# Optimization experiments

Hardware: AMD Instinct MI355X
Metric: run time of the kernel (lower is better)

## Reference

```python
import jax, jax.numpy as jnp
import numpy as np

K = 8
NUM_BLOCKS = 12

def knn_idx(xyz, k):
    # xyz: (B,3,N). kNN in Euclidean space (self included), like gutil.group.
    sq = jnp.sum(xyz * xyz, axis=1)                      # (B,N)
    inner = jnp.einsum('bdn,bdm->bnm', xyz, xyz)         # (B,N,N)
    dist = sq[:, :, None] - 2.0 * inner + sq[:, None, :]
    _, idx = jax.lax.top_k(-dist, k)                     # (B,N,k)
    return idx

def gather_neighbors(points, idx):
    # points: (B,d,N), idx: (B,N,k) -> grouped (B,d,k,N)  [gutil.group_point]
    g = jax.vmap(lambda p, i: p[:, i])(points, idx)      # (B,d,N,k)
    return jnp.transpose(g, (0, 1, 3, 2))

def setup_inputs() -> dict:
    key = jax.random.key(0)
    ks = jax.random.split(key, 6)
    B, N, D = 4, 4096, 128
    return {
        'xyz': jax.random.normal(ks[0], (B, 3, N), dtype=jnp.float32),
        'points': jax.random.normal(ks[1], (B, D, N), dtype=jnp.float32),
        'conv_w1': jax.random.normal(ks[2], (NUM_BLOCKS, D, D), dtype=jnp.float32) * 0.05,
        'conv_w2': jax.random.normal(ks[3], (NUM_BLOCKS, D, D), dtype=jnp.float32) * 0.05,
        'w_center': jax.random.normal(ks[4], (6, D), dtype=jnp.float32) * 0.05,
        'w_neighbor': jax.random.normal(ks[5], (6, D), dtype=jnp.float32) * 0.05,
    }

def reference(xyz, points, conv_w1, conv_w2, w_center, w_neighbor):
    # kNN indices depend only on xyz -> computed once (idx==0 branch in torch).
    idx = knn_idx(xyz, K)
    inv = 1.0 / (K + 1)
    for i in range(NUM_BLOCKS):
        shortcut = points
        p = jax.nn.relu(points)                              # (B,d,N)
        grouped = gather_neighbors(p, idx)                   # (B,d,K,N)
        center = jnp.einsum('oi,bin->bon', conv_w1[i], p)    # 1x1 conv on center
        gnn_sum = jnp.einsum('oi,bikn->bon', conv_w2[i], grouped)  # conv + sum over K
        # mean over concat([center(1), grouped(K)]) along neighbor dim + residual
        points = (center + gnn_sum) * inv + shortcut
        if i == NUM_BLOCKS - 1:
            pxyz = jnp.einsum('oi,bin->bon', w_center, p)            # (B,6,N)
            gxyz_sum = jnp.einsum('oi,bikn->bon', w_neighbor, grouped)
            new_xyz = (pxyz + gxyz_sum) * inv                        # (B,6,N)
            B, _, N = xyz.shape
            new_xyz = new_xyz.reshape(B, 3, 2, N) + xyz[:, :, None, :]
            new_xyz = new_xyz.reshape(B, 3, 2 * N)
            return (new_xyz, points)
```

## Files before the change

kernel.cpp:

```cpp
#include <hip/hip_runtime.h>
#include <math.h>

#define BB 4
#define NN 4096
#define DD 128
#define KK 8
#define NBLK 12

typedef __attribute__((ext_vector_type(8))) short short8;
typedef __attribute__((ext_vector_type(4))) float f32x4;

__device__ inline ushort bf16_rn(float x) {
    uint u = __float_as_uint(x);
    u = (u + 0x7FFFu + ((u >> 16) & 1u)) >> 16;
    return (ushort)u;
}
__device__ inline float bf16_f(ushort h) { return __uint_as_float(((uint)h) << 16); }

__global__ __launch_bounds__(512) void knn_kernel(const float* __restrict__ xyz,
                                                  int* __restrict__ idx) {
    __shared__ float xs[NN], ys[NN], zs[NN], sq[NN];
    const int b = blockIdx.y;
    const float* xb = xyz + (size_t)b * 3 * NN;
    for (int i = threadIdx.x; i < NN; i += 512) {
        float x = xb[i], y = xb[NN + i], z = xb[2 * NN + i];
        xs[i] = x; ys[i] = y; zs[i] = z;
        sq[i] = __fadd_rn(__fadd_rn(__fmul_rn(x, x), __fmul_rn(y, y)),
                          __fmul_rn(z, z));
    }
    __syncthreads();

    const int wave = threadIdx.x >> 6;
    const int lane = threadIdx.x & 63;
    const int n = blockIdx.x * 8 + wave;
    const float qx = xs[n], qy = ys[n], qz = zs[n], qsq = sq[n];

    float d[KK];
    int id[KK];
#pragma unroll
    for (int j = 0; j < KK; ++j) { d[j] = INFINITY; id[j] = -1; }

    for (int j = 0; j < NN / 256; ++j) {
        const int m0 = j * 256 + lane * 4;
        const float4 vx = *(const float4*)&xs[m0];
        const float4 vy = *(const float4*)&ys[m0];
        const float4 vz = *(const float4*)&zs[m0];
        const float4 vq = *(const float4*)&sq[m0];
#pragma unroll
        for (int e = 0; e < 4; ++e) {
            const float cx = (&vx.x)[e], cy = (&vy.x)[e], cz = (&vz.x)[e];
            const float cq = (&vq.x)[e];
            float inner = __fadd_rn(__fadd_rn(__fmul_rn(qx, cx),
                                              __fmul_rn(qy, cy)),
                                    __fmul_rn(qz, cz));
            float dist = __fadd_rn(__fsub_rn(qsq, __fmul_rn(2.0f, inner)), cq);
            if (dist < d[KK - 1]) {
                d[KK - 1] = dist; id[KK - 1] = m0 + e;
#pragma unroll
                for (int t = KK - 1; t > 0; --t) {
                    if (d[t] < d[t - 1]) {
                        float td = d[t]; d[t] = d[t - 1]; d[t - 1] = td;
                        int ti = id[t]; id[t] = id[t - 1]; id[t - 1] = ti;
                    }
                }
            }
        }
    }

    int out[KK];
#pragma unroll
    for (int it = 0; it < KK; ++it) {
        float hd = d[0];
        int hi = id[0];
#pragma unroll
        for (int s = 32; s; s >>= 1) {
            float od = __shfl_xor(hd, s, 64);
            int oi = __shfl_xor(hi, s, 64);
            if (od < hd || (od == hd && oi < hi)) { hd = od; hi = oi; }
        }
        out[it] = hi;
        if (hd == d[0] && hi == id[0]) {
#pragma unroll
            for (int t = 0; t < KK - 1; ++t) { d[t] = d[t + 1]; id[t] = id[t + 1]; }
            d[KK - 1] = INFINITY; id[KK - 1] = -1;
        }
    }

    if (lane == 0) {
        int* op = idx + ((size_t)b * NN + n) * KK;
        *(int4*)op       = make_int4(out[0], out[1], out[2], out[3]);
        *(int4*)(op + 4) = make_int4(out[4], out[5], out[6], out[7]);
    }
}

__global__ __launch_bounds__(256) void prep_w(const float* __restrict__ w1,
                                              const float* __restrict__ w2,
                                              ushort* __restrict__ whi,
                                              ushort* __restrict__ wlo) {
    const int e = blockIdx.x * 256 + threadIdx.x;
    const int l = e >> 15;
    const int rem = e & 32767;
    const int r = rem >> 8;
    const int k = rem & 255;
    float w = (k < 128) ? w1[((size_t)l * 128 + r) * 128 + k]
                        : w2[((size_t)l * 128 + r) * 128 + (k - 128)];
    ushort h = bf16_rn(w);
    whi[e] = h;
    wlo[e] = bf16_rn(w - bf16_f(h));
}

__global__ __launch_bounds__(256) void transpose_pts(const float* __restrict__ pts,
                                                     float* __restrict__ ptsT) {
    __shared__ float t[32][33];
    const int b = blockIdx.z;
    const int c0 = blockIdx.y * 32;
    const int n0 = blockIdx.x * 32;
    const int tx = threadIdx.x & 31;
    const int ty = threadIdx.x >> 5;
#pragma unroll
    for (int q = 0; q < 4; ++q)
        t[ty + 8 * q][tx] = pts[((size_t)b * DD + c0 + ty + 8 * q) * NN + n0 + tx];
    __syncthreads();
#pragma unroll
    for (int q = 0; q < 4; ++q)
        ptsT[((size_t)b * NN + n0 + ty + 8 * q) * DD + c0 + tx] = t[tx][ty + 8 * q];
}

__global__ __launch_bounds__(512, 4) void fused_block(const float* __restrict__ ptsT_in,
                                                      const int* __restrict__ idx,
                                                      const ushort* __restrict__ whi,
                                                      const ushort* __restrict__ wlo,
                                                      float* __restrict__ ptsT_out,
                                                      float* __restrict__ out_std,
                                                      const float* __restrict__ wc,
                                                      const float* __restrict__ wn,
                                                      const float* __restrict__ xyz,
                                                      float* __restrict__ out_xyz,
                                                      const int last) {
    __shared__ __align__(16) char xt[32768];
    __shared__ float sc[32][132];
    char* xt_hi = xt;
    char* xt_lo = xt + 16384;

    const int bid = blockIdx.x;
    const int xcd = bid & 7;
    const int b = xcd >> 1;
    const int colbase = (((xcd & 1) << 6) + (bid >> 3)) * 32;

    const int w = threadIdx.x >> 6;
    const int lane = threadIdx.x & 63;
    const int half = lane >> 5;
    const int l32 = lane & 31;
    const int choff = 4 * l32;
    const int row0 = w * 4;

    const float* baseT = ptsT_in + (size_t)b * NN * DD;

    const int iv = idx[((size_t)b * NN + colbase + row0) * KK + (lane & 31)];

    const int ln15 = lane & 15;
    const int kl = lane >> 4;

#pragma unroll
    for (int i = 0; i < 2; ++i) {
        const int n_loc = row0 + 2 * i + half;
        const int n = colbase + n_loc;

        int nb[KK];
#pragma unroll
        for (int j = 0; j < KK; ++j) nb[j] = __shfl(iv, (2 * i + half) * 8 + j, 64);

        const float4 c4 = *(const float4*)(baseT + (size_t)n * DD + choff);
        float4 u[KK];
#pragma unroll
        for (int j = 0; j < KK; ++j)
            u[j] = *(const float4*)(baseT + (size_t)nb[j] * DD + choff);

        float g0 = 0.f, g1 = 0.f, g2 = 0.f, g3 = 0.f;
#pragma unroll
        for (int j = 0; j < KK; ++j) {
            g0 += fmaxf(u[j].x, 0.f);
            g1 += fmaxf(u[j].y, 0.f);
            g2 += fmaxf(u[j].z, 0.f);
            g3 += fmaxf(u[j].w, 0.f);
        }
        const float p0 = fmaxf(c4.x, 0.f);
        const float p1 = fmaxf(c4.y, 0.f);
        const float p2 = fmaxf(c4.z, 0.f);
        const float p3 = fmaxf(c4.w, 0.f);

        *(float4*)&sc[n_loc][choff] = c4;

        ushort ph0 = bf16_rn(p0), ph1 = bf16_rn(p1), ph2 = bf16_rn(p2), ph3 = bf16_rn(p3);
        ushort pl0 = bf16_rn(p0 - bf16_f(ph0)), pl1 = bf16_rn(p1 - bf16_f(ph1));
        ushort pl2 = bf16_rn(p2 - bf16_f(ph2)), pl3 = bf16_rn(p3 - bf16_f(ph3));
        ushort gh0 = bf16_rn(g0), gh1 = bf16_rn(g1), gh2 = bf16_rn(g2), gh3 = bf16_rn(g3);
        ushort gl0 = bf16_rn(g0 - bf16_f(gh0)), gl1 = bf16_rn(g1 - bf16_f(gh1));
        ushort gl2 = bf16_rn(g2 - bf16_f(gh2)), gl3 = bf16_rn(g3 - bf16_f(gh3));

        const int gP = l32 >> 1;
        const int sub = (l32 & 1) << 3;
        const int byP = n_loc * 512 + ((gP ^ (n_loc & 7)) << 4) + sub;
        const int byG = n_loc * 512 + (((16 + gP) ^ (n_loc & 7)) << 4) + sub;

        *(unsigned long long*)(xt_hi + byP) =
            (unsigned long long)ph0 | ((unsigned long long)ph1 << 16) |
            ((unsigned long long)ph2 << 32) | ((unsigned long long)ph3 << 48);
        *(unsigned long long*)(xt_lo + byP) =
            (unsigned long long)pl0 | ((unsigned long long)pl1 << 16) |
            ((unsigned long long)pl2 << 32) | ((unsigned long long)pl3 << 48);
        *(unsigned long long*)(xt_hi + byG) =
            (unsigned long long)gh0 | ((unsigned long long)gh1 << 16) |
            ((unsigned long long)gh2 << 32) | ((unsigned long long)gh3 << 48);
        *(unsigned long long*)(xt_lo + byG) =
            (unsigned long long)gl0 | ((unsigned long long)gl1 << 16) |
            ((unsigned long long)gl2 << 32) | ((unsigned long long)gl3 << 48);

        if (last) {
            float s0, s1, s2, s3, s4, s5;
            {
                const int c0 = choff, c1 = choff + 1, c2 = choff + 2, c3 = choff + 3;
                s0 = p0 * wc[0 * 128 + c0] + p1 * wc[0 * 128 + c1] + p2 * wc[0 * 128 + c2] + p3 * wc[0 * 128 + c3]
                   + g0 * wn[0 * 128 + c0] + g1 * wn[0 * 128 + c1] + g2 * wn[0 * 128 + c2] + g3 * wn[0 * 128 + c3];
                s1 = p0 * wc[1 * 128 + c0] + p1 * wc[1 * 128 + c1] + p2 * wc[1 * 128 + c2] + p3 * wc[1 * 128 + c3]
                   + g0 * wn[1 * 128 + c0] + g1 * wn[1 * 128 + c1] + g2 * wn[1 * 128 + c2] + g3 * wn[1 * 128 + c3];
                s2 = p0 * wc[2 * 128 + c0] + p1 * wc[2 * 128 + c1] + p2 * wc[2 * 128 + c2] + p3 * wc[2 * 128 + c3]
                   + g0 * wn[2 * 128 + c0] + g1 * wn[2 * 128 + c1] + g2 * wn[2 * 128 + c2] + g3 * wn[2 * 128 + c3];
                s3 = p0 * wc[3 * 128 + c0] + p1 * wc[3 * 128 + c1] + p2 * wc[3 * 128 + c2] + p3 * wc[3 * 128 + c3]
                   + g0 * wn[3 * 128 + c0] + g1 * wn[3 * 128 + c1] + g2 * wn[3 * 128 + c2] + g3 * wn[3 * 128 + c3];
                s4 = p0 * wc[4 * 128 + c0] + p1 * wc[4 * 128 + c1] + p2 * wc[4 * 128 + c2] + p3 * wc[4 * 128 + c3]
                   + g0 * wn[4 * 128 + c0] + g1 * wn[4 * 128 + c1] + g2 * wn[4 * 128 + c2] + g3 * wn[4 * 128 + c3];
                s5 = p0 * wc[5 * 128 + c0] + p1 * wc[5 * 128 + c1] + p2 * wc[5 * 128 + c2] + p3 * wc[5 * 128 + c3]
                   + g0 * wn[5 * 128 + c0] + g1 * wn[5 * 128 + c1] + g2 * wn[5 * 128 + c2] + g3 * wn[5 * 128 + c3];
            }
#pragma unroll
            for (int st = 16; st; st >>= 1) {
                s0 += __shfl_xor(s0, st, 64);
                s1 += __shfl_xor(s1, st, 64);
                s2 += __shfl_xor(s2, st, 64);
                s3 += __shfl_xor(s3, st, 64);
                s4 += __shfl_xor(s4, st, 64);
                s5 += __shfl_xor(s5, st, 64);
            }
            if (l32 < 6) {
                float v = s0;
                v = (l32 == 1) ? s1 : v;
                v = (l32 == 2) ? s2 : v;
                v = (l32 == 3) ? s3 : v;
                v = (l32 == 4) ? s4 : v;
                v = (l32 == 5) ? s5 : v;
                const int dd = l32 >> 1, h = l32 & 1;
                const float xv = xyz[((size_t)b * 3 + dd) * NN + n];
                out_xyz[(((size_t)b * 3 + dd) * 2 + h) * NN + n] =
                    v * (1.0f / 9.0f) + xv;
            }
        }
    }
    __syncthreads();

    const int wrow = w * 16 + ln15;
    f32x4 acc[2] = {};
#pragma unroll
    for (int ks = 0; ks < 8; ++ks) {
        const short8 a_hi = *(const short8*)(whi + (size_t)wrow * 256 + ks * 32 + kl * 8);
        const short8 a_lo = *(const short8*)(wlo + (size_t)wrow * 256 + ks * 32 + kl * 8);
        short8 bfh[2], bfl[2];
#pragma unroll
        for (int nt = 0; nt < 2; ++nt) {
            const int n_loc = nt * 16 + ln15;
            const int by = n_loc * 512 + (((ks * 4 + kl) ^ (n_loc & 7)) << 4);
            bfh[nt] = *(const short8*)(xt_hi + by);
            bfl[nt] = *(const short8*)(xt_lo + by);
        }
#pragma unroll
        for (int nt = 0; nt < 2; ++nt) {
            acc[nt] = __builtin_amdgcn_mfma_f32_16x16x32_bf16(a_hi, bfh[nt], acc[nt], 0, 0, 0);
            acc[nt] = __builtin_amdgcn_mfma_f32_16x16x32_bf16(a_hi, bfl[nt], acc[nt], 0, 0, 0);
            acc[nt] = __builtin_amdgcn_mfma_f32_16x16x32_bf16(a_lo, bfh[nt], acc[nt], 0, 0, 0);
        }
    }

    const float inv = 1.0f / 9.0f;
    const int orow = w * 16 + kl * 4;
#pragma unroll
    for (int nt = 0; nt < 2; ++nt) {
        const int nl = nt * 16 + ln15;
        const int n = colbase + nl;
        const float4 scv = *(const float4*)&sc[nl][orow];
        float v0 = acc[nt][0] * inv + scv.x;
        float v1 = acc[nt][1] * inv + scv.y;
        float v2 = acc[nt][2] * inv + scv.z;
        float v3 = acc[nt][3] * inv + scv.w;
        if (!last) {
            *(float4*)(ptsT_out + ((size_t)b * NN + n) * DD + orow) =
                make_float4(v0, v1, v2, v3);
        } else {
            out_std[((size_t)b * DD + orow + 0) * NN + n] = v0;
            out_std[((size_t)b * DD + orow + 1) * NN + n] = v1;
            out_std[((size_t)b * DD + orow + 2) * NN + n] = v2;
            out_std[((size_t)b * DD + orow + 3) * NN + n] = v3;
        }
    }
}

extern "C" void kernel_launch(void* const* d_in, const int* in_sizes, int n_in,
                              void* d_out, int out_size, void* d_ws, size_t ws_size,
                              hipStream_t stream) {
    const float* xyz    = (const float*)d_in[0];
    const float* points = (const float*)d_in[1];
    const float* w1     = (const float*)d_in[2];
    const float* w2     = (const float*)d_in[3];
    const float* wc     = (const float*)d_in[4];
    const float* wn     = (const float*)d_in[5];
    float* out = (float*)d_out;

    const size_t feat = (size_t)BB * DD * NN;
    char* ws = (char*)d_ws;
    int*    idx  = (int*)ws;
    ushort* whi  = (ushort*)(ws + 524288);
    ushort* wlo  = (ushort*)(ws + 524288 + 786432);
    float*  pT0  = (float*)(ws + 524288 + 2 * 786432);
    float*  pT1  = pT0 + feat;

    knn_kernel<<<dim3(NN / 8, BB), 512, 0, stream>>>(xyz, idx);
    prep_w<<<dim3(12 * 128 * 256 / 256), 256, 0, stream>>>(w1, w2, whi, wlo);
    transpose_pts<<<dim3(NN / 32, DD / 32, BB), 256, 0, stream>>>(points, pT0);

    float* out_pts = out + (size_t)BB * 3 * 2 * NN;
    float* bufs[2] = {pT0, pT1};
    for (int i = 0; i < NBLK; ++i) {
        const int last = (i == NBLK - 1);
        fused_block<<<dim3(512), 512, 0, stream>>>(
            bufs[i & 1], idx, whi + (size_t)i * 32768, wlo + (size_t)i * 32768,
            bufs[(i + 1) & 1], out_pts, wc, wn, xyz, out, last);
    }
}
```

Measured before the change: 296.3 us.

## Reorder points by Morton code so kNN gathers hit nearby rows

Adds a per-batch Morton-code bitonic sort of the points, then permutes the feature rows and the remapped kNN indices into spatial order. The 12 fused blocks then run in that order, and the final outputs are scattered back to original positions through the permutation. The aim is better cache locality for the neighbour gathers, since spatially close points now sit in nearby memory. In exchange it adds a single-block-per-batch sort, two permute kernels, an extra workspace buffer and non-coalesced scattered stores in the last block.

Result: slower. 325.6 us (+9.9%).

```diff
diff --git a/kernel.cpp b/kernel.cpp
--- a/kernel.cpp
+++ b/kernel.cpp
@@ -91,6 +91,75 @@
         *(int4*)op       = make_int4(out[0], out[1], out[2], out[3]);
         *(int4*)(op + 4) = make_int4(out[4], out[5], out[6], out[7]);
     }
+}
+
+__device__ inline uint expand10(uint v) {
+    v &= 0x3FFu;
+    v = (v | (v << 16)) & 0x030000FFu;
+    v = (v | (v << 8))  & 0x0300F00Fu;
+    v = (v | (v << 4))  & 0x030C30C3u;
+    v = (v | (v << 2))  & 0x09249249u;
+    return v;
+}
+
+__global__ __launch_bounds__(1024) void morton_sort(const float* __restrict__ xyz,
+                                                    int* __restrict__ perm,
+                                                    int* __restrict__ inv) {
+    __shared__ unsigned long long a[NN];
+    const int b = blockIdx.x;
+    const float* xb = xyz + (size_t)b * 3 * NN;
+    for (int i = threadIdx.x; i < NN; i += 1024) {
+        float x = xb[i], y = xb[NN + i], z = xb[2 * NN + i];
+        uint qx = (uint)fminf(fmaxf((x + 4.f) * 128.f, 0.f), 1023.f);
+        uint qy = (uint)fminf(fmaxf((y + 4.f) * 128.f, 0.f), 1023.f);
+        uint qz = (uint)fminf(fmaxf((z + 4.f) * 128.f, 0.f), 1023.f);
+        uint code = (expand10(qx) << 2) | (expand10(qy) << 1) | expand10(qz);
+        a[i] = ((unsigned long long)code << 32) | (uint)i;
+    }
+    __syncthreads();
+    for (int k = 2; k <= NN; k <<= 1) {
+        for (int j = k >> 1; j > 0; j >>= 1) {
+            for (int t = threadIdx.x; t < NN / 2; t += 1024) {
+                const int i = ((t & ~(j - 1)) << 1) | (t & (j - 1));
+                const int l = i | j;
+                const bool up = ((i & k) == 0);
+                unsigned long long ai = a[i], al = a[l];
+                if ((ai > al) == up) { a[i] = al; a[l] = ai; }
+            }
+            __syncthreads();
+        }
+    }
+    for (int i = threadIdx.x; i < NN; i += 1024) {
+        const int orig = (int)(a[i] & 0xFFFFFFFFu);
+        perm[b * NN + i] = orig;
+        inv[b * NN + orig] = i;
+    }
+}
+
+__global__ __launch_bounds__(256) void permute_idx(const int* __restrict__ idx,
+                                                   const int* __restrict__ perm,
+                                                   const int* __restrict__ inv,
+                                                   int* __restrict__ idxp) {
+    const int b = blockIdx.y;
+    const int n = blockIdx.x * 256 + threadIdx.x;
+    const int orig = perm[b * NN + n];
+    const int* src = idx + ((size_t)b * NN + orig) * KK;
+    const int* invb = inv + b * NN;
+    int* dst = idxp + ((size_t)b * NN + n) * KK;
+#pragma unroll
+    for (int k = 0; k < KK; ++k) dst[k] = invb[src[k]];
+}
+
+__global__ __launch_bounds__(256) void permute_rows(const float* __restrict__ src,
+                                                    const int* __restrict__ perm,
+                                                    float* __restrict__ dst) {
+    const int b = blockIdx.y;
+    const int w = threadIdx.x >> 6;
+    const int lane = threadIdx.x & 63;
+    const int n = blockIdx.x * 4 + w;
+    const int orig = perm[b * NN + n];
+    const float2 v = *(const float2*)(src + ((size_t)b * NN + orig) * DD + 2 * lane);
+    *(float2*)(dst + ((size_t)b * NN + n) * DD + 2 * lane) = v;
 }
 
 __global__ __launch_bounds__(256) void prep_w(const float* __restrict__ w1,
@@ -127,7 +196,7 @@
 }
 
 __global__ __launch_bounds__(512, 4) void fused_block(const float* __restrict__ ptsT_in,
-                                                      const int* __restrict__ idx,
+                                                      const int* __restrict__ idxp,
                                                       const ushort* __restrict__ whi,
                                                       const ushort* __restrict__ wlo,
                                                       float* __restrict__ ptsT_out,
@@ -136,6 +205,7 @@
                                                       const float* __restrict__ wn,
                                                       const float* __restrict__ xyz,
                                                       float* __restrict__ out_xyz,
+                                                      const int* __restrict__ perm,
                                                       const int last) {
     __shared__ __align__(16) char xt[32768];
     __shared__ float sc[32][132];
@@ -156,7 +226,7 @@
 
     const float* baseT = ptsT_in + (size_t)b * NN * DD;
 
-    const int iv = idx[((size_t)b * NN + colbase + row0) * KK + (lane & 31)];
+    const int iv = idxp[((size_t)b * NN + colbase + row0) * KK + (lane & 31)];
 
     const int ln15 = lane & 15;
     const int kl = lane >> 4;
@@ -249,9 +319,10 @@
                 v = (l32 == 3) ? s3 : v;
                 v = (l32 == 4) ? s4 : v;
                 v = (l32 == 5) ? s5 : v;
+                const int norig = perm[b * NN + n];
                 const int dd = l32 >> 1, h = l32 & 1;
-                const float xv = xyz[((size_t)b * 3 + dd) * NN + n];
-                out_xyz[(((size_t)b * 3 + dd) * 2 + h) * NN + n] =
+                const float xv = xyz[((size_t)b * 3 + dd) * NN + norig];
+                out_xyz[(((size_t)b * 3 + dd) * 2 + h) * NN + norig] =
                     v * (1.0f / 9.0f) + xv;
             }
         }
@@ -295,10 +366,11 @@
             *(float4*)(ptsT_out + ((size_t)b * NN + n) * DD + orow) =
                 make_float4(v0, v1, v2, v3);
         } else {
-            out_std[((size_t)b * DD + orow + 0) * NN + n] = v0;
-            out_std[((size_t)b * DD + orow + 1) * NN + n] = v1;
-            out_std[((size_t)b * DD + orow + 2) * NN + n] = v2;
-            out_std[((size_t)b * DD + orow + 3) * NN + n] = v3;
+            const int norig = perm[b * NN + n];
+            out_std[((size_t)b * DD + orow + 0) * NN + norig] = v0;
+            out_std[((size_t)b * DD + orow + 1) * NN + norig] = v1;
+            out_std[((size_t)b * DD + orow + 2) * NN + norig] = v2;
+            out_std[((size_t)b * DD + orow + 3) * NN + norig] = v3;
         }
     }
 }
@@ -316,22 +388,29 @@
 
     const size_t feat = (size_t)BB * DD * NN;
     char* ws = (char*)d_ws;
-    int*    idx  = (int*)ws;
-    ushort* whi  = (ushort*)(ws + 524288);
-    ushort* wlo  = (ushort*)(ws + 524288 + 786432);
-    float*  pT0  = (float*)(ws + 524288 + 2 * 786432);
-    float*  pT1  = pT0 + feat;
+    int*    idx   = (int*)(ws + 0);
+    int*    idxp  = (int*)(ws + 524288);
+    int*    perm  = (int*)(ws + 1048576);
+    int*    inv   = (int*)(ws + 1114112);
+    ushort* whi   = (ushort*)(ws + 1179648);
+    ushort* wlo   = (ushort*)(ws + 1966080);
+    float*  pT0   = (float*)(ws + 2752512);
+    float*  pT1   = pT0 + feat;
+    float*  pTt   = pT1 + feat;
 
     knn_kernel<<<dim3(NN / 8, BB), 512, 0, stream>>>(xyz, idx);
+    morton_sort<<<dim3(BB), 1024, 0, stream>>>(xyz, perm, inv);
     prep_w<<<dim3(12 * 128 * 256 / 256), 256, 0, stream>>>(w1, w2, whi, wlo);
-    transpose_pts<<<dim3(NN / 32, DD / 32, BB), 256, 0, stream>>>(points, pT0);
+    transpose_pts<<<dim3(NN / 32, DD / 32, BB), 256, 0, stream>>>(points, pTt);
+    permute_rows<<<dim3(NN / 4, BB), 256, 0, stream>>>(pTt, perm, pT0);
+    permute_idx<<<dim3(NN / 256, BB), 256, 0, stream>>>(idx, perm, inv, idxp);
 
     float* out_pts = out + (size_t)BB * 3 * 2 * NN;
     float* bufs[2] = {pT0, pT1};
     for (int i = 0; i < NBLK; ++i) {
         const int last = (i == NBLK - 1);
         fused_block<<<dim3(512), 512, 0, stream>>>(
-            bufs[i & 1], idx, whi + (size_t)i * 32768, wlo + (size_t)i * 32768,
-            bufs[(i + 1) & 1], out_pts, wc, wn, xyz, out, last);
-    }
-}
+            bufs[i & 1], idxp, whi + (size_t)i * 32768, wlo + (size_t)i * 32768,
+            bufs[(i + 1) & 1], out_pts, wc, wn, xyz, out, perm, last);
+    }
+}
```

## Halve fused block column tile to 16 and recompute squared norms in kNN

Applied to the files above, without the earlier changes.

Each fused_block workgroup now covers 16 points instead of 32, so the grid doubles to 1024 workgroups and LDS use per workgroup halves. Each workgroup does one gather iteration and one MFMA column tile instead of two. The aim is more parallelism and occupancy across the GPU, at the cost of reloading the per-block weight fragments twice as often. Separately, the kNN kernel drops the shared squared-norm array and recomputes the norms in the inner loop, trading extra ALU work for less LDS traffic.

After: 346.5 us. 17.0% more time.

```diff
diff --git a/kernel.cpp b/kernel.cpp
--- a/kernel.cpp
+++ b/kernel.cpp
@@ -19,21 +19,22 @@
 
 __global__ __launch_bounds__(512) void knn_kernel(const float* __restrict__ xyz,
                                                   int* __restrict__ idx) {
-    __shared__ float xs[NN], ys[NN], zs[NN], sq[NN];
+    __shared__ float xs[NN], ys[NN], zs[NN];
     const int b = blockIdx.y;
     const float* xb = xyz + (size_t)b * 3 * NN;
     for (int i = threadIdx.x; i < NN; i += 512) {
-        float x = xb[i], y = xb[NN + i], z = xb[2 * NN + i];
-        xs[i] = x; ys[i] = y; zs[i] = z;
-        sq[i] = __fadd_rn(__fadd_rn(__fmul_rn(x, x), __fmul_rn(y, y)),
-                          __fmul_rn(z, z));
+        xs[i] = xb[i];
+        ys[i] = xb[NN + i];
+        zs[i] = xb[2 * NN + i];
     }
     __syncthreads();
 
     const int wave = threadIdx.x >> 6;
     const int lane = threadIdx.x & 63;
     const int n = blockIdx.x * 8 + wave;
-    const float qx = xs[n], qy = ys[n], qz = zs[n], qsq = sq[n];
+    const float qx = xs[n], qy = ys[n], qz = zs[n];
+    const float qsq = __fadd_rn(__fadd_rn(__fmul_rn(qx, qx), __fmul_rn(qy, qy)),
+                                __fmul_rn(qz, qz));
 
     float d[KK];
     int id[KK];
@@ -45,11 +46,12 @@
         const float4 vx = *(const float4*)&xs[m0];
         const float4 vy = *(const float4*)&ys[m0];
         const float4 vz = *(const float4*)&zs[m0];
-        const float4 vq = *(const float4*)&sq[m0];
 #pragma unroll
         for (int e = 0; e < 4; ++e) {
             const float cx = (&vx.x)[e], cy = (&vy.x)[e], cz = (&vz.x)[e];
-            const float cq = (&vq.x)[e];
+            const float cq = __fadd_rn(__fadd_rn(__fmul_rn(cx, cx),
+                                                 __fmul_rn(cy, cy)),
+                                       __fmul_rn(cz, cz));
             float inner = __fadd_rn(__fadd_rn(__fmul_rn(qx, cx),
                                               __fmul_rn(qy, cy)),
                                     __fmul_rn(qz, cz));
@@ -137,38 +139,37 @@
                                                       const float* __restrict__ xyz,
                                                       float* __restrict__ out_xyz,
                                                       const int last) {
-    __shared__ __align__(16) char xt[32768];
-    __shared__ float sc[32][132];
+    __shared__ __align__(16) char xt[16384];
+    __shared__ float sc[16][132];
     char* xt_hi = xt;
-    char* xt_lo = xt + 16384;
+    char* xt_lo = xt + 8192;
 
     const int bid = blockIdx.x;
     const int xcd = bid & 7;
     const int b = xcd >> 1;
-    const int colbase = (((xcd & 1) << 6) + (bid >> 3)) * 32;
+    const int colbase = (((xcd & 1) << 7) + (bid >> 3)) * 16;
 
     const int w = threadIdx.x >> 6;
     const int lane = threadIdx.x & 63;
     const int half = lane >> 5;
     const int l32 = lane & 31;
     const int choff = 4 * l32;
-    const int row0 = w * 4;
+    const int row0 = w * 2;
 
     const float* baseT = ptsT_in + (size_t)b * NN * DD;
 
-    const int iv = idx[((size_t)b * NN + colbase + row0) * KK + (lane & 31)];
+    const int iv = idx[((size_t)b * NN + colbase + row0) * KK + (lane & 15)];
 
     const int ln15 = lane & 15;
     const int kl = lane >> 4;
 
-#pragma unroll
-    for (int i = 0; i < 2; ++i) {
-        const int n_loc = row0 + 2 * i + half;
+    {
+        const int n_loc = row0 + half;
         const int n = colbase + n_loc;
 
         int nb[KK];
 #pragma unroll
-        for (int j = 0; j < KK; ++j) nb[j] = __shfl(iv, (2 * i + half) * 8 + j, 64);
+        for (int j = 0; j < KK; ++j) nb[j] = __shfl(iv, half * 8 + j, 64);
 
         const float4 c4 = *(const float4*)(baseT + (size_t)n * DD + choff);
         float4 u[KK];
@@ -259,38 +260,29 @@
     __syncthreads();
 
     const int wrow = w * 16 + ln15;
-    f32x4 acc[2] = {};
+    f32x4 acc = {};
 #pragma unroll
     for (int ks = 0; ks < 8; ++ks) {
         const short8 a_hi = *(const short8*)(whi + (size_t)wrow * 256 + ks * 32 + kl * 8);
         const short8 a_lo = *(const short8*)(wlo + (size_t)wrow * 256 + ks * 32 + kl * 8);
-        short8 bfh[2], bfl[2];
-#pragma unroll
-        for (int nt = 0; nt < 2; ++nt) {
-            const int n_loc = nt * 16 + ln15;
-            const int by = n_loc * 512 + (((ks * 4 + kl) ^ (n_loc & 7)) << 4);
-            bfh[nt] = *(const short8*)(xt_hi + by);
-            bfl[nt] = *(const short8*)(xt_lo + by);
-        }
-#pragma unroll
-        for (int nt = 0; nt < 2; ++nt) {
-            acc[nt] = __builtin_amdgcn_mfma_f32_16x16x32_bf16(a_hi, bfh[nt], acc[nt], 0, 0, 0);
-            acc[nt] = __builtin_amdgcn_mfma_f32_16x16x32_bf16(a_hi, bfl[nt], acc[nt], 0, 0, 0);
-            acc[nt] = __builtin_amdgcn_mfma_f32_16x16x32_bf16(a_lo, bfh[nt], acc[nt], 0, 0, 0);
-        }
+        const int by = ln15 * 512 + (((ks * 4 + kl) ^ (ln15 & 7)) << 4);
+        const short8 bfh = *(const short8*)(xt_hi + by);
+        const short8 bfl = *(const short8*)(xt_lo + by);
+        acc = __builtin_amdgcn_mfma_f32_16x16x32_bf16(a_hi, bfh, acc, 0, 0, 0);
+        acc = __builtin_amdgcn_mfma_f32_16x16x32_bf16(a_hi, bfl, acc, 0, 0, 0);
+        acc = __builtin_amdgcn_mfma_f32_16x16x32_bf16(a_lo, bfh, acc, 0, 0, 0);
     }
 
     const float inv = 1.0f / 9.0f;
     const int orow = w * 16 + kl * 4;
-#pragma unroll
-    for (int nt = 0; nt < 2; ++nt) {
-        const int nl = nt * 16 + ln15;
+    {
+        const int nl = ln15;
         const int n = colbase + nl;
         const float4 scv = *(const float4*)&sc[nl][orow];
-        float v0 = acc[nt][0] * inv + scv.x;
-        float v1 = acc[nt][1] * inv + scv.y;
-        float v2 = acc[nt][2] * inv + scv.z;
-        float v3 = acc[nt][3] * inv + scv.w;
+        float v0 = acc[0] * inv + scv.x;
+        float v1 = acc[1] * inv + scv.y;
+        float v2 = acc[2] * inv + scv.z;
+        float v3 = acc[3] * inv + scv.w;
         if (!last) {
             *(float4*)(ptsT_out + ((size_t)b * NN + n) * DD + orow) =
                 make_float4(v0, v1, v2, v3);
@@ -330,7 +322,7 @@
     float* bufs[2] = {pT0, pT1};
     for (int i = 0; i < NBLK; ++i) {
         const int last = (i == NBLK - 1);
-        fused_block<<<dim3(512), 512, 0, stream>>>(
+        fused_block<<<dim3(1024), 512, 0, stream>>>(
             bufs[i & 1], idx, whi + (size_t)i * 32768, wlo + (size_t)i * 32768,
             bufs[(i + 1) & 1], out_pts, wc, wn, xyz, out, last);
     }
```
